# Kernel tuning notes

Measured on AMD Instinct MI355X. Metric: run time of the kernel, lower is better.

## Reference

```python
import jax, jax.numpy as jnp
import numpy as np

B, L, D = 4096, 64, 128
NUM_IDS = 1000


def setup_inputs() -> dict:
    key = jax.random.key(0)
    ks = jax.random.split(key, 8)
    src_node_ids = jax.random.randint(ks[0], (B,), 0, NUM_IDS, dtype=jnp.int32)
    dst_node_ids = jax.random.randint(ks[1], (B,), 0, NUM_IDS, dtype=jnp.int32)
    src_nb = jax.random.randint(ks[2], (B, L), 0, NUM_IDS, dtype=jnp.int32)
    dst_nb = jax.random.randint(ks[3], (B, L), 0, NUM_IDS, dtype=jnp.int32)
    # MLP params: Linear(1 -> D), ReLU, Linear(D -> D)
    W1 = jax.random.normal(ks[4], (1, D), dtype=jnp.float32) / jnp.sqrt(1.0)
    b1 = jnp.zeros((D,), dtype=jnp.float32)
    W2 = jax.random.normal(ks[5], (D, D), dtype=jnp.float32) / jnp.sqrt(D)
    b2 = jnp.zeros((D,), dtype=jnp.float32)
    return {
        "src_node_ids": src_node_ids,
        "dst_node_ids": dst_node_ids,
        "src_nodes_neighbor_ids": src_nb,
        "dst_nodes_neighbor_ids": dst_nb,
        "W1": W1, "b1": b1, "W2": W2, "b2": b2,
    }


def _appearances(src_id, dst_id, src_nb, dst_nb):
    # counts of each neighbor within its own list: (B, L)
    c_src = (src_nb[:, :, None] == src_nb[:, None, :]).sum(-1)
    c_dst = (dst_nb[:, :, None] == dst_nb[:, None, :]).sum(-1)
    # cross counts: count of src neighbor in dst list and vice versa
    c_dst_of_src = (src_nb[:, :, None] == dst_nb[:, None, :]).sum(-1)  # (B, L)
    c_src_of_dst = (dst_nb[:, :, None] == src_nb[:, None, :]).sum(-1)  # (B, L)
    # scalar per batch: count of src_id in dst list, dst_id in src list
    cd_srcid = (dst_nb == src_id[:, None]).sum(-1)  # (B,)
    cs_dstid = (src_nb == dst_id[:, None]).sum(-1)  # (B,)
    srcid_in_dst = cd_srcid > 0
    same = src_id == dst_id
    # dict-mutation semantics of count_nodes_appearances:
    # src_mapping[src_id] overwritten with cd_srcid when src_id in dst list
    # dst_mapping[dst_id] overwritten with (post-mutation) src_mapping[dst_id]
    cond2 = (cs_dstid > 0) | (same & srcid_in_dst)
    v2 = jnp.where(same & srcid_in_dst, cd_srcid, cs_dstid)
    # dst_mapping.get(src neighbors): count in dst, with dst_id override
    src_col1 = jnp.where((src_nb == dst_id[:, None]) & cond2[:, None],
                         v2[:, None], c_dst_of_src)
    # src_mapping.get(dst neighbors): count in src, with src_id override
    dst_col0 = jnp.where((dst_nb == src_id[:, None]) & srcid_in_dst[:, None],
                         cd_srcid[:, None], c_src_of_dst)
    src_app = jnp.stack([c_src, src_col1], axis=-1).astype(jnp.float32)  # (B,L,2)
    dst_app = jnp.stack([dst_col0, c_dst], axis=-1).astype(jnp.float32)  # (B,L,2)
    return src_app, dst_app


def _mlp(app, W1, b1, W2, b2):
    # app: (B, L, 2) -> (B, L, 2, D) -> sum over the 2 co-occurrence channels
    h = jax.nn.relu(app[..., None] * W1[0] + b1)      # (B, L, 2, D)
    out = jnp.einsum('blcd,de->blce', h, W2) + b2     # (B, L, 2, D)
    return out.sum(axis=2)                            # (B, L, D)


def reference(src_node_ids, dst_node_ids, src_nodes_neighbor_ids,
              dst_nodes_neighbor_ids, W1, b1, W2, b2):
    src_app, dst_app = _appearances(src_node_ids, dst_node_ids,
                                    src_nodes_neighbor_ids, dst_nodes_neighbor_ids)
    src_feat = _mlp(src_app, W1, b1, W2, b2)
    dst_feat = _mlp(dst_app, W1, b1, W2, b2)
    return src_feat, dst_feat
```

## Files before the change

kernel.cpp:

```cpp
#include <hip/hip_runtime.h>

#define DD   128
#define LLEN 64
#define TMAX 65
#define ROWS_PER_BLK 4
#define TAB4 (TMAX * (DD / 4))

__global__ void build_table_kernel(const float* __restrict__ W1,
                                   const float* __restrict__ b1,
                                   const float* __restrict__ W2,
                                   const float* __restrict__ b2,
                                   float* __restrict__ tab) {
    const int a = blockIdx.x;
    const int e = threadIdx.x;
    const float fa = (float)a;
    float acc = b2[e];
#pragma unroll 8
    for (int d = 0; d < DD; ++d) {
        float h = fmaxf(fmaf(fa, W1[d], b1[d]), 0.f);
        acc = fmaf(h, W2[d * DD + e], acc);
    }
    tab[a * DD + e] = acc;
}

__global__ __launch_bounds__(256) void nif_main_kernel(
    const int* __restrict__ src_id, const int* __restrict__ dst_id,
    const int* __restrict__ src_nb, const int* __restrict__ dst_nb,
    const float* __restrict__ tab, float* __restrict__ out, int B) {
    __shared__ float4 TAB[TAB4];
    __shared__ int S[ROWS_PER_BLK][LLEN], Dn[ROWS_PER_BLK][LLEN];
    __shared__ int A0[ROWS_PER_BLK][LLEN], A1[ROWS_PER_BLK][LLEN];
    __shared__ int C0[ROWS_PER_BLK][LLEN], C1[ROWS_PER_BLK][LLEN];

    const int tid  = threadIdx.x;
    const int w    = tid >> 6;
    const int lane = tid & 63;
    const int b    = blockIdx.x * ROWS_PER_BLK + w;

    const float4* __restrict__ tabg = (const float4*)tab;
#pragma unroll
    for (int i = tid; i < TAB4; i += 256) TAB[i] = tabg[i];

    S[w][lane]  = src_nb[(size_t)b * LLEN + lane];
    Dn[w][lane] = dst_nb[(size_t)b * LLEN + lane];
    __syncthreads();

    {
        const int sid = src_id[b];
        const int did = dst_id[b];
        const int vs = S[w][lane];
        const int vd = Dn[w][lane];
        const int cd_sid = __popcll(__ballot(vd == sid));
        const int cs_did = __popcll(__ballot(vs == did));
        int c_src = 0, c_dos = 0, c_dst = 0, c_sod = 0;
#pragma unroll 8
        for (int j = 0; j < LLEN; ++j) {
            const int sj = S[w][j], dj = Dn[w][j];
            c_src += (sj == vs);
            c_dos += (dj == vs);
            c_dst += (dj == vd);
            c_sod += (sj == vd);
        }
        const bool s_in_d = (cd_sid > 0);
        const bool same   = (sid == did);
        const bool c2     = (cs_did > 0) || (same && s_in_d);
        const int  v2     = (same && s_in_d) ? cd_sid : cs_did;
        A0[w][lane] = c_src;
        A1[w][lane] = (vs == did && c2) ? v2 : c_dos;
        C0[w][lane] = (vd == sid && s_in_d) ? cd_sid : c_sod;
        C1[w][lane] = c_dst;
    }
    __syncthreads();

    float4* __restrict__ out4 = (float4*)out;
    const size_t src_base = (size_t)b * (LLEN * DD / 4);
    const size_t dst_base = src_base + (size_t)B * (LLEN * DD / 4);
    const int e4 = lane & 31;
    const int lh = lane >> 5;
#pragma unroll 4
    for (int k = 0; k < 32; ++k) {
        const int l = 2 * k + lh;
        const int idx4 = l * 32 + e4;
        const float4 t0 = TAB[A0[w][l] * 32 + e4];
        const float4 t1 = TAB[A1[w][l] * 32 + e4];
        float4 v;
        v.x = t0.x + t1.x;
        v.y = t0.y + t1.y;
        v.z = t0.z + t1.z;
        v.w = t0.w + t1.w;
        out4[src_base + idx4] = v;
        const float4 u0 = TAB[C0[w][l] * 32 + e4];
        const float4 u1 = TAB[C1[w][l] * 32 + e4];
        float4 wv;
        wv.x = u0.x + u1.x;
        wv.y = u0.y + u1.y;
        wv.z = u0.z + u1.z;
        wv.w = u0.w + u1.w;
        out4[dst_base + idx4] = wv;
    }
}

extern "C" void kernel_launch(void* const* d_in, const int* in_sizes, int n_in,
                              void* d_out, int out_size, void* d_ws, size_t ws_size,
                              hipStream_t stream) {
    const int*   src_id = (const int*)d_in[0];
    const int*   dst_id = (const int*)d_in[1];
    const int*   src_nb = (const int*)d_in[2];
    const int*   dst_nb = (const int*)d_in[3];
    const float* W1     = (const float*)d_in[4];
    const float* b1     = (const float*)d_in[5];
    const float* W2     = (const float*)d_in[6];
    const float* b2     = (const float*)d_in[7];
    float*       out    = (float*)d_out;
    float*       tab    = (float*)d_ws;

    const int B = in_sizes[0];

    build_table_kernel<<<TMAX, DD, 0, stream>>>(W1, b1, W2, b2, tab);
    nif_main_kernel<<<B / ROWS_PER_BLK, 256, 0, stream>>>(
        src_id, dst_id, src_nb, dst_nb, tab, out, B);
}
```

Measured before the change: 278.5 us.

## Use wave shuffles instead of LDS for counts and use nontemporal output stores

Neighbor ids and the computed counts now stay in registers and are broadcast with wave shuffles, so the per-row LDS arrays and one barrier are gone. The output loop is restructured so each half-wave writes either the src or the dst output for every l, using nontemporal stores to keep the large write stream from polluting cache. It also adds an occupancy hint to the launch bounds and unrolls the table copy into LDS. Shuffles cost ALU/DS bandwidth, and the memory-bound output store stream likely dominates anyway.

```diff
diff --git a/kernel.cpp b/kernel.cpp
--- a/kernel.cpp
+++ b/kernel.cpp
@@ -5,6 +5,8 @@
 #define TMAX 65
 #define ROWS_PER_BLK 4
 #define TAB4 (TMAX * (DD / 4))
+
+typedef __attribute__((ext_vector_type(4))) float f32x4;
 
 __global__ void build_table_kernel(const float* __restrict__ W1,
                                    const float* __restrict__ b1,
@@ -23,80 +25,67 @@
     tab[a * DD + e] = acc;
 }
 
-__global__ __launch_bounds__(256) void nif_main_kernel(
+__global__ __launch_bounds__(256, 4) void nif_main_kernel(
     const int* __restrict__ src_id, const int* __restrict__ dst_id,
     const int* __restrict__ src_nb, const int* __restrict__ dst_nb,
     const float* __restrict__ tab, float* __restrict__ out, int B) {
-    __shared__ float4 TAB[TAB4];
-    __shared__ int S[ROWS_PER_BLK][LLEN], Dn[ROWS_PER_BLK][LLEN];
-    __shared__ int A0[ROWS_PER_BLK][LLEN], A1[ROWS_PER_BLK][LLEN];
-    __shared__ int C0[ROWS_PER_BLK][LLEN], C1[ROWS_PER_BLK][LLEN];
+    __shared__ f32x4 TAB[TAB4];
 
     const int tid  = threadIdx.x;
+    const int lane = tid & 63;
     const int w    = tid >> 6;
-    const int lane = tid & 63;
     const int b    = blockIdx.x * ROWS_PER_BLK + w;
 
-    const float4* __restrict__ tabg = (const float4*)tab;
+    const int vs  = src_nb[(size_t)b * LLEN + lane];
+    const int vd  = dst_nb[(size_t)b * LLEN + lane];
+    const int sid = src_id[b];
+    const int did = dst_id[b];
+
+    const f32x4* __restrict__ tabg = (const f32x4*)tab;
 #pragma unroll
-    for (int i = tid; i < TAB4; i += 256) TAB[i] = tabg[i];
+    for (int i = 0; i < 8; ++i) TAB[tid + 256 * i] = tabg[tid + 256 * i];
+    if (tid < TAB4 - 2048) TAB[2048 + tid] = tabg[2048 + tid];
 
-    S[w][lane]  = src_nb[(size_t)b * LLEN + lane];
-    Dn[w][lane] = dst_nb[(size_t)b * LLEN + lane];
+    int c_src = 0, c_dos = 0, c_dst = 0, c_sod = 0;
+#pragma unroll 8
+    for (int j = 0; j < LLEN; ++j) {
+        const int sj = __shfl(vs, j);
+        const int dj = __shfl(vd, j);
+        c_src += (sj == vs);
+        c_dos += (dj == vs);
+        c_dst += (dj == vd);
+        c_sod += (sj == vd);
+    }
+    const int cd_sid = __popcll(__ballot(vd == sid));
+    const int cs_did = __popcll(__ballot(vs == did));
+    const bool s_in_d = (cd_sid > 0);
+    const bool same   = (sid == did);
+    const bool c2     = (cs_did > 0) || (same && s_in_d);
+    const int  v2     = (same && s_in_d) ? cd_sid : cs_did;
+    const int A0 = c_src;
+    const int A1 = (vs == did && c2) ? v2 : c_dos;
+    const int C0 = (vd == sid && s_in_d) ? cd_sid : c_sod;
+    const int C1 = c_dst;
+
     __syncthreads();
 
-    {
-        const int sid = src_id[b];
-        const int did = dst_id[b];
-        const int vs = S[w][lane];
-        const int vd = Dn[w][lane];
-        const int cd_sid = __popcll(__ballot(vd == sid));
-        const int cs_did = __popcll(__ballot(vs == did));
-        int c_src = 0, c_dos = 0, c_dst = 0, c_sod = 0;
-#pragma unroll 8
-        for (int j = 0; j < LLEN; ++j) {
-            const int sj = S[w][j], dj = Dn[w][j];
-            c_src += (sj == vs);
-            c_dos += (dj == vs);
-            c_dst += (dj == vd);
-            c_sod += (sj == vd);
-        }
-        const bool s_in_d = (cd_sid > 0);
-        const bool same   = (sid == did);
-        const bool c2     = (cs_did > 0) || (same && s_in_d);
-        const int  v2     = (same && s_in_d) ? cd_sid : cs_did;
-        A0[w][lane] = c_src;
-        A1[w][lane] = (vs == did && c2) ? v2 : c_dos;
-        C0[w][lane] = (vd == sid && s_in_d) ? cd_sid : c_sod;
-        C1[w][lane] = c_dst;
-    }
-    __syncthreads();
-
-    float4* __restrict__ out4 = (float4*)out;
+    const int e4 = lane & 31;
+    const int lh = lane >> 5;
     const size_t src_base = (size_t)b * (LLEN * DD / 4);
     const size_t dst_base = src_base + (size_t)B * (LLEN * DD / 4);
-    const int e4 = lane & 31;
-    const int lh = lane >> 5;
+    f32x4* __restrict__ myout =
+        (f32x4*)out + (lh ? dst_base : src_base) + e4;
+
 #pragma unroll 4
-    for (int k = 0; k < 32; ++k) {
-        const int l = 2 * k + lh;
-        const int idx4 = l * 32 + e4;
-        const float4 t0 = TAB[A0[w][l] * 32 + e4];
-        const float4 t1 = TAB[A1[w][l] * 32 + e4];
-        float4 v;
-        v.x = t0.x + t1.x;
-        v.y = t0.y + t1.y;
-        v.z = t0.z + t1.z;
-        v.w = t0.w + t1.w;
-        out4[src_base + idx4] = v;
-        const float4 u0 = TAB[C0[w][l] * 32 + e4];
-        const float4 u1 = TAB[C1[w][l] * 32 + e4];
-        float4 wv;
-        wv.x = u0.x + u1.x;
-        wv.y = u0.y + u1.y;
-        wv.z = u0.z + u1.z;
-        wv.w = u0.w + u1.w;
-        out4[dst_base + idx4] = wv;
+    for (int l = 0; l < LLEN; ++l) {
+        const int a0 = __shfl(A0, l);
+        const int a1 = __shfl(A1, l);
+        const int c0 = __shfl(C0, l);
+        const int c1 = __shfl(C1, l);
+        const int p = lh ? c0 : a0;
+        const int q = lh ? c1 : a1;
+        const f32x4 t = TAB[p * 32 + e4] + TAB[q * 32 + e4];
+        __builtin_nontemporal_store(t, myout + (size_t)l * 32);
     }
 }
 
```

Measured after the change: 290.2 us. 4.2% more time.
